# Kernel tuning notes

Hardware: AMD Instinct MI355X
Metric: run time of the kernel (lower is better)

Reference implementation:

```python
import jax, jax.numpy as jnp
import numpy as np

NNZ = 16777216  # 2**24 nonzeros
D = 2048        # dense size (D, D, D); sum over dim 2 -> (D, D)


def setup_inputs() -> dict:
    key = jax.random.key(0)
    kv, ki = jax.random.split(key)
    values = jax.random.normal(kv, (NNZ,), dtype=jnp.float32)
    indices = jax.random.randint(ki, (3, NNZ), 0, D, dtype=jnp.int64)
    return {"values": values, "indices": indices}


def reference(values, indices):
    # sparse_coo_tensor(indices, values, size=(D,D,D)) -> sparse.sum(dim=2) -> to_dense()
    # is equivalent to a scatter-add of values keyed by (indices[0], indices[1]):
    # the third index only distinguishes entries that get summed away, and COO
    # coalescing already sums duplicate coordinates.
    out = jnp.zeros((D, D), dtype=jnp.float32)
    out = out.at[indices[0], indices[1]].add(values)
    return out
```

## Files before the change

### kernel.cpp

```cpp
#include <hip/hip_runtime.h>

#define NNZ 16777216
#define D 2048
#define NB 512
#define ROWS_PER_B 4
#define CAP 35840u
#define K1_BLOCK 512
#define K1_EPT 16
#define K1_CHUNK (K1_BLOCK * K1_EPT)
#define K1_VEC (K1_EPT / 4)

__global__ void init_cursors(unsigned int* __restrict__ cursor) {
    int i = threadIdx.x;
    if (i < NB) cursor[i] = (unsigned int)i * CAP;
}

__global__ __launch_bounds__(K1_BLOCK) void bin_scatter(
    const float* __restrict__ values,
    const int* __restrict__ idx0,
    const int* __restrict__ idx1,
    unsigned int* __restrict__ bins,
    unsigned int* __restrict__ cursor)
{
    __shared__ unsigned int lhist[NB];
    __shared__ unsigned int sprefix[NB];
    __shared__ unsigned int sgbase[NB];
    __shared__ unsigned int wsum[8];
    __shared__ unsigned int skey[K1_CHUNK];
    __shared__ unsigned short sval[K1_CHUNK];

    const int tid = threadIdx.x;
    lhist[tid] = 0;
    __syncthreads();

    const int vecBase = blockIdx.x * (K1_CHUNK / 4);

    float4 v[K1_VEC]; int4 a[K1_VEC]; int4 c[K1_VEC];
#pragma unroll
    for (int it = 0; it < K1_VEC; ++it) {
        int g = vecBase + it * K1_BLOCK + tid;
        v[it] = reinterpret_cast<const float4*>(values)[g];
        a[it] = reinterpret_cast<const int4*>(idx0)[g];
        c[it] = reinterpret_cast<const int4*>(idx1)[g];
    }

    unsigned short rank[K1_EPT];
#pragma unroll
    for (int it = 0; it < K1_VEC; ++it) {
        const int* ap = reinterpret_cast<const int*>(&a[it]);
#pragma unroll
        for (int e = 0; e < 4; ++e)
            rank[it * 4 + e] = (unsigned short)atomicAdd(&lhist[ap[e] >> 2], 1u);
    }
    __syncthreads();

    {
        const int lane = tid & 63;
        const int wid = tid >> 6;
        unsigned int cnt = lhist[tid];
        unsigned int x = cnt;
#pragma unroll
        for (int dlt = 1; dlt < 64; dlt <<= 1) {
            unsigned int y = __shfl_up(x, dlt, 64);
            if (lane >= dlt) x += y;
        }
        if (lane == 63) wsum[wid] = x;
        sgbase[tid] = cnt ? atomicAdd(&cursor[tid], cnt) : 0u;
        __syncthreads();
        unsigned int off = 0;
#pragma unroll
        for (int wjj = 0; wjj < 8; ++wjj) off += (wjj < wid) ? wsum[wjj] : 0u;
        sprefix[tid] = x - cnt + off;
    }
    __syncthreads();

#pragma unroll
    for (int it = 0; it < K1_VEC; ++it) {
        const int*   ap = reinterpret_cast<const int*>(&a[it]);
        const int*   cp = reinterpret_cast<const int*>(&c[it]);
        const float* vp = reinterpret_cast<const float*>(&v[it]);
#pragma unroll
        for (int e = 0; e < 4; ++e) {
            int i0 = ap[e], i1 = cp[e];
            unsigned int slot = sprefix[i0 >> 2] + rank[it * 4 + e];
            unsigned int fb = __float_as_uint(vp[e]);
            skey[slot] = ((unsigned int)i0 << 11) | (unsigned int)i1;
            sval[slot] = (unsigned short)((fb + 0x7fffu + ((fb >> 16) & 1u)) >> 16);
        }
    }
    __syncthreads();

#pragma unroll
    for (int it = 0; it < K1_EPT; ++it) {
        int s = it * K1_BLOCK + tid;
        unsigned int k = skey[s];
        unsigned int b = k >> 13;
        unsigned int addr = sgbase[b] + ((unsigned int)s - sprefix[b]);
        if (addr < (b + 1) * CAP)
            bins[addr] = ((k & 0x1FFFu) << 16) | (unsigned int)sval[s];
    }
}

__global__ __launch_bounds__(1024) void bucket_accumulate(
    const unsigned int* __restrict__ bins,
    const unsigned int* __restrict__ cursor,
    float* __restrict__ out)
{
    __shared__ float tile[ROWS_PER_B * D];

    const int b = blockIdx.x;
    const int tid = threadIdx.x;

    for (int j = tid; j < ROWS_PER_B * D / 4; j += 1024)
        reinterpret_cast<float4*>(tile)[j] = make_float4(0.f, 0.f, 0.f, 0.f);
    __syncthreads();

    const unsigned int base = (unsigned int)b * CAP;
    unsigned int n = cursor[b] - base;
    if (n > CAP) n = CAP;

    const uint4* b4 = reinterpret_cast<const uint4*>(bins + base);
    const unsigned int nv = n >> 2;
    for (unsigned int i = tid; i < nv; i += 1024) {
        uint4 p = b4[i];
        atomicAdd(&tile[p.x >> 16], __uint_as_float(p.x << 16));
        atomicAdd(&tile[p.y >> 16], __uint_as_float(p.y << 16));
        atomicAdd(&tile[p.z >> 16], __uint_as_float(p.z << 16));
        atomicAdd(&tile[p.w >> 16], __uint_as_float(p.w << 16));
    }
    for (unsigned int i = (nv << 2) + tid; i < n; i += 1024) {
        unsigned int p = bins[base + i];
        atomicAdd(&tile[p >> 16], __uint_as_float(p << 16));
    }
    __syncthreads();

    float4* o4 = reinterpret_cast<float4*>(out + (size_t)b * ROWS_PER_B * D);
    for (int j = tid; j < ROWS_PER_B * D / 4; j += 1024)
        o4[j] = reinterpret_cast<float4*>(tile)[j];
}

__global__ __launch_bounds__(256) void scatter_add_kernel(
    const float* __restrict__ values,
    const int* __restrict__ idx0,
    const int* __restrict__ idx1,
    float* __restrict__ out)
{
    const int nvec = NNZ / 4;
    int tid = blockIdx.x * blockDim.x + threadIdx.x;
    int stride = gridDim.x * blockDim.x;
    for (int i = tid; i < nvec; i += stride) {
        const float4 v = reinterpret_cast<const float4*>(values)[i];
        const int4   a = reinterpret_cast<const int4*>(idx0)[i];
        const int4   b = reinterpret_cast<const int4*>(idx1)[i];
        atomicAdd(&out[a.x * D + b.x], v.x);
        atomicAdd(&out[a.y * D + b.y], v.y);
        atomicAdd(&out[a.z * D + b.z], v.z);
        atomicAdd(&out[a.w * D + b.w], v.w);
    }
}

extern "C" void kernel_launch(void* const* d_in, const int* in_sizes, int n_in,
                              void* d_out, int out_size, void* d_ws, size_t ws_size,
                              hipStream_t stream) {
    const float* values  = (const float*)d_in[0];
    const int*   indices = (const int*)d_in[1];
    const int*   idx0 = indices;
    const int*   idx1 = indices + NNZ;
    float* out = (float*)d_out;

    const size_t need = 4096 + (size_t)NB * CAP * sizeof(unsigned int);

    if (ws_size < need) {
        hipMemsetAsync(out, 0, (size_t)out_size * sizeof(float), stream);
        const int nvec = NNZ / 4;
        scatter_add_kernel<<<(nvec + 255) / 256, 256, 0, stream>>>(values, idx0, idx1, out);
        return;
    }

    unsigned int* cursor = (unsigned int*)d_ws;
    unsigned int* bins   = (unsigned int*)((char*)d_ws + 4096);

    init_cursors<<<1, NB, 0, stream>>>(cursor);
    bin_scatter<<<NNZ / K1_CHUNK, K1_BLOCK, 0, stream>>>(values, idx0, idx1, bins, cursor);
    bucket_accumulate<<<NB, 1024, 0, stream>>>(bins, cursor, out);
}
```

Measured before the change: 163.4 us.

## Replicate bin cursors across sixteen sub-segments to cut global atomic contention

Splits each of the 512 row-bins into 16 sub-segments chosen by block index, so the scatter blocks do their global cursor atomics on 16 separate counter sets instead of one. The scatter kernel moves to 1024-thread blocks handling 8 elements per thread, and the cursor init kernel is replaced by a memset. The accumulate kernel uses 512 threads and reads the 16 sub-segments, issuing the first load of each up front for more memory-level parallelism. The cost is a per-sub-segment capacity limit (2560), which risks silently dropping entries if one overflows, plus scattered reads across segments in the second kernel.

```diff
diff --git a/kernel.cpp b/kernel.cpp
--- a/kernel.cpp
+++ b/kernel.cpp
@@ -4,18 +4,16 @@
 #define D 2048
 #define NB 512
 #define ROWS_PER_B 4
-#define CAP 35840u
-#define K1_BLOCK 512
-#define K1_EPT 16
+#define R 16
+#define CAPR 2560u
+#define CAPT (R * CAPR)
+#define K1_BLOCK 1024
+#define K1_EPT 8
 #define K1_CHUNK (K1_BLOCK * K1_EPT)
 #define K1_VEC (K1_EPT / 4)
-
-__global__ void init_cursors(unsigned int* __restrict__ cursor) {
-    int i = threadIdx.x;
-    if (i < NB) cursor[i] = (unsigned int)i * CAP;
-}
-
-__global__ __launch_bounds__(K1_BLOCK) void bin_scatter(
+#define K2_BLOCK 512
+
+__global__ __launch_bounds__(K1_BLOCK, 8) void bin_scatter(
     const float* __restrict__ values,
     const int* __restrict__ idx0,
     const int* __restrict__ idx1,
@@ -30,7 +28,8 @@
     __shared__ unsigned short sval[K1_CHUNK];
 
     const int tid = threadIdx.x;
-    lhist[tid] = 0;
+    const unsigned int r = (unsigned int)blockIdx.x & (R - 1);
+    if (tid < NB) lhist[tid] = 0;
     __syncthreads();
 
     const int vecBase = blockIdx.x * (K1_CHUNK / 4);
@@ -54,19 +53,22 @@
     }
     __syncthreads();
 
-    {
+    unsigned int x = 0, cnt = 0;
+    if (tid < NB) {
         const int lane = tid & 63;
-        const int wid = tid >> 6;
-        unsigned int cnt = lhist[tid];
-        unsigned int x = cnt;
+        cnt = lhist[tid];
+        x = cnt;
 #pragma unroll
         for (int dlt = 1; dlt < 64; dlt <<= 1) {
             unsigned int y = __shfl_up(x, dlt, 64);
             if (lane >= dlt) x += y;
         }
-        if (lane == 63) wsum[wid] = x;
-        sgbase[tid] = cnt ? atomicAdd(&cursor[tid], cnt) : 0u;
-        __syncthreads();
+        if (lane == 63) wsum[tid >> 6] = x;
+        sgbase[tid] = cnt ? atomicAdd(&cursor[r * NB + tid], cnt) : 0u;
+    }
+    __syncthreads();
+    if (tid < NB) {
+        const int wid = tid >> 6;
         unsigned int off = 0;
 #pragma unroll
         for (int wjj = 0; wjj < 8; ++wjj) off += (wjj < wid) ? wsum[wjj] : 0u;
@@ -95,13 +97,13 @@
         int s = it * K1_BLOCK + tid;
         unsigned int k = skey[s];
         unsigned int b = k >> 13;
-        unsigned int addr = sgbase[b] + ((unsigned int)s - sprefix[b]);
-        if (addr < (b + 1) * CAP)
-            bins[addr] = ((k & 0x1FFFu) << 16) | (unsigned int)sval[s];
-    }
-}
-
-__global__ __launch_bounds__(1024) void bucket_accumulate(
+        unsigned int rel = sgbase[b] + ((unsigned int)s - sprefix[b]);
+        if (rel < CAPR)
+            bins[b * CAPT + r * CAPR + rel] = ((k & 0x1FFFu) << 16) | (unsigned int)sval[s];
+    }
+}
+
+__global__ __launch_bounds__(K2_BLOCK, 4) void bucket_accumulate(
     const unsigned int* __restrict__ bins,
     const unsigned int* __restrict__ cursor,
     float* __restrict__ out)
@@ -111,31 +113,57 @@
     const int b = blockIdx.x;
     const int tid = threadIdx.x;
 
-    for (int j = tid; j < ROWS_PER_B * D / 4; j += 1024)
+    for (int j = tid; j < ROWS_PER_B * D / 4; j += K2_BLOCK)
         reinterpret_cast<float4*>(tile)[j] = make_float4(0.f, 0.f, 0.f, 0.f);
     __syncthreads();
 
-    const unsigned int base = (unsigned int)b * CAP;
-    unsigned int n = cursor[b] - base;
-    if (n > CAP) n = CAP;
-
-    const uint4* b4 = reinterpret_cast<const uint4*>(bins + base);
-    const unsigned int nv = n >> 2;
-    for (unsigned int i = tid; i < nv; i += 1024) {
-        uint4 p = b4[i];
-        atomicAdd(&tile[p.x >> 16], __uint_as_float(p.x << 16));
-        atomicAdd(&tile[p.y >> 16], __uint_as_float(p.y << 16));
-        atomicAdd(&tile[p.z >> 16], __uint_as_float(p.z << 16));
-        atomicAdd(&tile[p.w >> 16], __uint_as_float(p.w << 16));
-    }
-    for (unsigned int i = (nv << 2) + tid; i < n; i += 1024) {
-        unsigned int p = bins[base + i];
-        atomicAdd(&tile[p >> 16], __uint_as_float(p << 16));
+    unsigned int n[R];
+#pragma unroll
+    for (int rr = 0; rr < R; ++rr) {
+        unsigned int t = cursor[rr * NB + b];
+        n[rr] = t > CAPR ? CAPR : t;
+    }
+
+    const uint4* b4 = reinterpret_cast<const uint4*>(bins);
+    uint4 p[R];
+    unsigned int msk = 0;
+#pragma unroll
+    for (int rr = 0; rr < R; ++rr) {
+        unsigned int nv = n[rr] >> 2;
+        unsigned int seg4 = (unsigned int)b * (CAPT / 4) + (unsigned int)rr * (CAPR / 4);
+        if ((unsigned int)tid < nv) { p[rr] = b4[seg4 + tid]; msk |= 1u << rr; }
+    }
+#pragma unroll
+    for (int rr = 0; rr < R; ++rr) {
+        if (msk & (1u << rr)) {
+            atomicAdd(&tile[p[rr].x >> 16], __uint_as_float(p[rr].x << 16));
+            atomicAdd(&tile[p[rr].y >> 16], __uint_as_float(p[rr].y << 16));
+            atomicAdd(&tile[p[rr].z >> 16], __uint_as_float(p[rr].z << 16));
+            atomicAdd(&tile[p[rr].w >> 16], __uint_as_float(p[rr].w << 16));
+        }
+    }
+
+#pragma unroll
+    for (int rr = 0; rr < R; ++rr) {
+        unsigned int nv = n[rr] >> 2;
+        unsigned int seg4 = (unsigned int)b * (CAPT / 4) + (unsigned int)rr * (CAPR / 4);
+        for (unsigned int i = (unsigned int)tid + K2_BLOCK; i < nv; i += K2_BLOCK) {
+            uint4 q = b4[seg4 + i];
+            atomicAdd(&tile[q.x >> 16], __uint_as_float(q.x << 16));
+            atomicAdd(&tile[q.y >> 16], __uint_as_float(q.y << 16));
+            atomicAdd(&tile[q.z >> 16], __uint_as_float(q.z << 16));
+            atomicAdd(&tile[q.w >> 16], __uint_as_float(q.w << 16));
+        }
+        unsigned int rem = n[rr] & 3u;
+        if ((unsigned int)tid < rem) {
+            unsigned int w = bins[(seg4 << 2) + (nv << 2) + tid];
+            atomicAdd(&tile[w >> 16], __uint_as_float(w << 16));
+        }
     }
     __syncthreads();
 
     float4* o4 = reinterpret_cast<float4*>(out + (size_t)b * ROWS_PER_B * D);
-    for (int j = tid; j < ROWS_PER_B * D / 4; j += 1024)
+    for (int j = tid; j < ROWS_PER_B * D / 4; j += K2_BLOCK)
         o4[j] = reinterpret_cast<float4*>(tile)[j];
 }
 
@@ -168,7 +196,8 @@
     const int*   idx1 = indices + NNZ;
     float* out = (float*)d_out;
 
-    const size_t need = 4096 + (size_t)NB * CAP * sizeof(unsigned int);
+    const size_t cur_bytes = (size_t)R * NB * sizeof(unsigned int);
+    const size_t need = cur_bytes + (size_t)NB * CAPT * sizeof(unsigned int);
 
     if (ws_size < need) {
         hipMemsetAsync(out, 0, (size_t)out_size * sizeof(float), stream);
@@ -178,9 +207,9 @@
     }
 
     unsigned int* cursor = (unsigned int*)d_ws;
-    unsigned int* bins   = (unsigned int*)((char*)d_ws + 4096);
-
-    init_cursors<<<1, NB, 0, stream>>>(cursor);
+    unsigned int* bins   = (unsigned int*)((char*)d_ws + cur_bytes);
+
+    hipMemsetAsync(cursor, 0, cur_bytes, stream);
     bin_scatter<<<NNZ / K1_CHUNK, K1_BLOCK, 0, stream>>>(values, idx0, idx1, bins, cursor);
-    bucket_accumulate<<<NB, 1024, 0, stream>>>(bins, cursor, out);
-}
+    bucket_accumulate<<<NB, K2_BLOCK, 0, stream>>>(bins, cursor, out);
+}
```

Result: faster. 156.4 us (-4.3%).
